# Kernel optimization log

Hardware: AMD Instinct MI355X
Metric: run time of the kernel (lower is better)

## Reference

```python
import jax, jax.numpy as jnp
import numpy as np

ALPHA = 0.9
BETA = 0.1
GAMMA = 0.1
EPS = 1e-8  # torch cosine_similarity eps


def setup_inputs() -> dict:
    key = jax.random.key(0)
    k1, k2 = jax.random.split(key)
    N = 8192
    y = jax.random.normal(k1, (N, 1), dtype=jnp.float32)
    labels = jax.random.normal(k2, (N, 1), dtype=jnp.float32)
    return {"y": y, "labels": labels}


def reference(y, labels):
    # --- MSE ---
    mse_loss = jnp.mean((y - labels) ** 2)

    # --- cosine similarity along dim=1 (torch semantics: each norm clamped by eps) ---
    yn = jnp.linalg.norm(y, axis=1)        # [N]
    ln = jnp.linalg.norm(labels, axis=1)   # [N]
    cos = jnp.sum(y * labels, axis=1) / (jnp.maximum(yn, EPS) * jnp.maximum(ln, EPS))
    similarity_loss = 1.0 - jnp.mean(cos)

    # --- vectorized pairwise margin ranking over i<j ---
    ys = y[:, 0]       # [N]
    ls = labels[:, 0]  # [N]
    dy = ys[:, None] - ys[None, :]   # [N, N]
    dl = ls[:, None] - ls[None, :]   # [N, N]
    # r_ij = 1 if labels[i] > labels[j], -1 if <, else sign(y[i]-y[j])
    r = jnp.where(dl > 0, 1.0, jnp.where(dl < 0, -1.0, jnp.sign(dy)))
    N = ys.shape[0]
    upper = jnp.triu(jnp.ones((N, N), dtype=bool), k=1)  # i<j pairs
    hinge = jnp.maximum(0.0, -r * dy)
    margin_ranking_loss = jnp.sum(jnp.where(upper, hinge, 0.0)) / (N * (N - 1) / 2)

    return ALPHA * mse_loss + BETA * margin_ranking_loss + GAMMA * similarity_loss
```

## Files before the change

kernel.cpp:

```cpp
#include <hip/hip_runtime.h>
#include <hip/hip_bf16.h>


constexpr int BLOCK = 256;
constexpr int JT    = 32;

#define EPS_F 1e-8f

__global__ __launch_bounds__(BLOCK) void combined_loss_pair_kernel(
    const float* __restrict__ y, const float* __restrict__ l, int N,
    float* __restrict__ hpart,
    float* __restrict__ mpart,
    float* __restrict__ cpart)
{
    __shared__ float sy[BLOCK];
    __shared__ float sl[BLOCK];
    __shared__ float red[BLOCK / 64];

    const int bx  = blockIdx.x;
    const int it  = bx / JT;
    const int jt  = bx % JT;
    const int tid = threadIdx.x;

    const int i    = it * BLOCK + tid;
    const bool valid = (i < N);
    const float yi = valid ? y[i] : 0.f;
    const float li = valid ? l[i] : 0.f;

    const int chunk = (N + JT - 1) / JT;
    const int j0 = jt * chunk;
    const int j1 = min(N, j0 + chunk);

    float hsum = 0.f;
    for (int jb = j0; jb < j1; jb += BLOCK) {
        const int cnt = min(BLOCK, j1 - jb);
        if (tid < cnt) {
            sy[tid] = y[jb + tid];
            sl[tid] = l[jb + tid];
        }
        __syncthreads();
        if (valid) {
#pragma unroll 8
            for (int k = 0; k < cnt; ++k) {
                const float dl = li - sl[k];
                const float dy = yi - sy[k];
                const float c = (dl > 0.f) ? fmaxf(-dy, 0.f)
                              : ((dl < 0.f) ? fmaxf(dy, 0.f) : 0.f);
                hsum += c;
            }
        }
        __syncthreads();
    }

    for (int o = 32; o > 0; o >>= 1) hsum += __shfl_down(hsum, o, 64);
    const int lane = tid & 63, wid = tid >> 6;
    if (lane == 0) red[wid] = hsum;
    __syncthreads();
    if (tid == 0) {
        float s = 0.f;
        for (int w = 0; w < BLOCK / 64; ++w) s += red[w];
        hpart[bx] = s;
    }
    __syncthreads();

    if (jt == 0) {
        float m = 0.f, c = 0.f;
        if (valid) {
            const float d = yi - li;
            m = d * d;
            c = (yi * li) / (fmaxf(fabsf(yi), EPS_F) * fmaxf(fabsf(li), EPS_F));
        }
        for (int o = 32; o > 0; o >>= 1) {
            m += __shfl_down(m, o, 64);
            c += __shfl_down(c, o, 64);
        }
        if (lane == 0) red[wid] = m;
        __syncthreads();
        float msum = 0.f;
        if (tid == 0) for (int w = 0; w < BLOCK / 64; ++w) msum += red[w];
        __syncthreads();
        if (lane == 0) red[wid] = c;
        __syncthreads();
        if (tid == 0) {
            float csum = 0.f;
            for (int w = 0; w < BLOCK / 64; ++w) csum += red[w];
            mpart[it] = msum;
            cpart[it] = csum;
        }
    }
}

__global__ __launch_bounds__(256) void combined_loss_finalize_kernel(
    const float* __restrict__ hpart, const float* __restrict__ mpart,
    const float* __restrict__ cpart, int nh, int nm, int N,
    float* __restrict__ out)
{
    double h = 0.0, m = 0.0, c = 0.0;
    for (int k = threadIdx.x; k < nh; k += blockDim.x) h += (double)hpart[k];
    for (int k = threadIdx.x; k < nm; k += blockDim.x) {
        m += (double)mpart[k];
        c += (double)cpart[k];
    }
    for (int o = 32; o > 0; o >>= 1) {
        h += __shfl_down(h, o, 64);
        m += __shfl_down(m, o, 64);
        c += __shfl_down(c, o, 64);
    }
    __shared__ double sh[4][3];
    const int lane = threadIdx.x & 63, wid = threadIdx.x >> 6;
    if (lane == 0) { sh[wid][0] = h; sh[wid][1] = m; sh[wid][2] = c; }
    __syncthreads();
    if (threadIdx.x == 0) {
        double H = 0, M = 0, C = 0;
        for (int w = 0; w < 4; ++w) { H += sh[w][0]; M += sh[w][1]; C += sh[w][2]; }
        const double Nd = (double)N;
        const double mse    = M / Nd;
        const double pairs  = Nd * (Nd - 1.0) * 0.5;
        const double margin = (H * 0.5) / pairs;
        const double sim    = 1.0 - C / Nd;
        out[0] = (float)(0.9 * mse + 0.1 * margin + 0.1 * sim);
    }
}

extern "C" void kernel_launch(void* const* d_in, const int* in_sizes, int n_in,
                              void* d_out, int out_size, void* d_ws, size_t ws_size,
                              hipStream_t stream) {
    const float* y = (const float*)d_in[0];
    const float* l = (const float*)d_in[1];
    const int N = in_sizes[0];

    const int IT = (N + BLOCK - 1) / BLOCK;
    float* hpart = (float*)d_ws;
    float* mpart = hpart + (size_t)IT * JT;
    float* cpart = mpart + IT;

    combined_loss_pair_kernel<<<IT * JT, BLOCK, 0, stream>>>(y, l, N, hpart, mpart, cpart);
    combined_loss_finalize_kernel<<<1, 256, 0, stream>>>(hpart, mpart, cpart, IT * JT, IT, N,
                                                         (float*)d_out);
}
```

Measured before the change: 82.24 us.

## Rewrite pairwise hinge as abs/sign sum and register-tile four rows per thread

Each hinge term is rewritten branch-free as 0.5*(|dy| + s*dy), where the sign s comes from comparing the labels. The two pieces are accumulated separately and combined once per row. Each thread now holds four i-rows in registers, and each block processes a 64-element j chunk read from LDS as float4, so every shared-memory load serves four rows. The aim is to cut per-pair ALU and LDS traffic while keeping about the same block count. The cost is more registers per thread, and exactly tied label pairs with i != j are handled slightly differently from the reference.

New measurement: 68.50 us. 16.7% less time.

```diff
diff --git a/kernel.cpp b/kernel.cpp
--- a/kernel.cpp
+++ b/kernel.cpp
@@ -3,18 +3,20 @@
 
 
 constexpr int BLOCK = 256;
-constexpr int JT    = 32;
+constexpr int M_PER = 4;
+constexpr int ITILE = BLOCK * M_PER;
+constexpr int JCH   = 64;
 
 #define EPS_F 1e-8f
 
 __global__ __launch_bounds__(BLOCK) void combined_loss_pair_kernel(
-    const float* __restrict__ y, const float* __restrict__ l, int N,
+    const float* __restrict__ y, const float* __restrict__ l, int N, int JT,
     float* __restrict__ hpart,
     float* __restrict__ mpart,
     float* __restrict__ cpart)
 {
-    __shared__ float sy[BLOCK];
-    __shared__ float sl[BLOCK];
+    __shared__ float sy[JCH];
+    __shared__ float sl[JCH];
     __shared__ float red[BLOCK / 64];
 
     const int bx  = blockIdx.x;
@@ -22,39 +24,60 @@
     const int jt  = bx % JT;
     const int tid = threadIdx.x;
 
-    const int i    = it * BLOCK + tid;
-    const bool valid = (i < N);
-    const float yi = valid ? y[i] : 0.f;
-    const float li = valid ? l[i] : 0.f;
-
-    const int chunk = (N + JT - 1) / JT;
-    const int j0 = jt * chunk;
-    const int j1 = min(N, j0 + chunk);
-
-    float hsum = 0.f;
-    for (int jb = j0; jb < j1; jb += BLOCK) {
-        const int cnt = min(BLOCK, j1 - jb);
-        if (tid < cnt) {
-            sy[tid] = y[jb + tid];
-            sl[tid] = l[jb + tid];
-        }
-        __syncthreads();
-        if (valid) {
-#pragma unroll 8
-            for (int k = 0; k < cnt; ++k) {
-                const float dl = li - sl[k];
-                const float dy = yi - sy[k];
-                const float c = (dl > 0.f) ? fmaxf(-dy, 0.f)
-                              : ((dl < 0.f) ? fmaxf(dy, 0.f) : 0.f);
-                hsum += c;
-            }
-        }
-        __syncthreads();
+    float yi[M_PER], li[M_PER];
+    bool  vm[M_PER];
+#pragma unroll
+    for (int m = 0; m < M_PER; ++m) {
+        const int i = it * ITILE + m * BLOCK + tid;
+        vm[m] = (i < N);
+        yi[m] = vm[m] ? y[i] : 0.f;
+        li[m] = vm[m] ? l[i] : 0.f;
     }
 
-    for (int o = 32; o > 0; o >>= 1) hsum += __shfl_down(hsum, o, 64);
+    const int j0   = jt * JCH;
+    const int jcnt = min(JCH, N - j0);
+    if (tid < JCH) {
+        const bool vj = (tid < jcnt);
+        sy[tid] = vj ? y[j0 + tid] : 0.f;
+        sl[tid] = vj ? l[j0 + tid] : 0.f;
+    }
+    __syncthreads();
+
+    float A[M_PER], B[M_PER];
+#pragma unroll
+    for (int m = 0; m < M_PER; ++m) { A[m] = 0.f; B[m] = 0.f; }
+
+#define PROC(yj, lj)                                         \
+    {                                                        \
+        _Pragma("unroll")                                    \
+        for (int m = 0; m < M_PER; ++m) {                    \
+            const float u = yi[m] - (yj);                    \
+            A[m] += fabsf(u);                                \
+            B[m] += (li[m] < (lj)) ? u : -u;                 \
+        }                                                    \
+    }
+
+    const int kv = jcnt & ~3;
+#pragma unroll 4
+    for (int k = 0; k < kv; k += 4) {
+        const float4 y4 = *reinterpret_cast<const float4*>(&sy[k]);
+        const float4 l4 = *reinterpret_cast<const float4*>(&sl[k]);
+        PROC(y4.x, l4.x);
+        PROC(y4.y, l4.y);
+        PROC(y4.z, l4.z);
+        PROC(y4.w, l4.w);
+    }
+    for (int k = kv; k < jcnt; ++k) PROC(sy[k], sl[k]);
+#undef PROC
+
+    float h = 0.f;
+#pragma unroll
+    for (int m = 0; m < M_PER; ++m)
+        if (vm[m]) h += 0.5f * (A[m] + B[m]);
+
+    for (int o = 32; o > 0; o >>= 1) h += __shfl_down(h, o, 64);
     const int lane = tid & 63, wid = tid >> 6;
-    if (lane == 0) red[wid] = hsum;
+    if (lane == 0) red[wid] = h;
     __syncthreads();
     if (tid == 0) {
         float s = 0.f;
@@ -64,28 +87,32 @@
     __syncthreads();
 
     if (jt == 0) {
-        float m = 0.f, c = 0.f;
-        if (valid) {
-            const float d = yi - li;
-            m = d * d;
-            c = (yi * li) / (fmaxf(fabsf(yi), EPS_F) * fmaxf(fabsf(li), EPS_F));
+        float msum = 0.f, csum = 0.f;
+#pragma unroll
+        for (int m = 0; m < M_PER; ++m) {
+            if (vm[m]) {
+                const float d = yi[m] - li[m];
+                msum += d * d;
+                csum += (yi[m] * li[m]) /
+                        (fmaxf(fabsf(yi[m]), EPS_F) * fmaxf(fabsf(li[m]), EPS_F));
+            }
         }
         for (int o = 32; o > 0; o >>= 1) {
-            m += __shfl_down(m, o, 64);
-            c += __shfl_down(c, o, 64);
+            msum += __shfl_down(msum, o, 64);
+            csum += __shfl_down(csum, o, 64);
         }
-        if (lane == 0) red[wid] = m;
+        if (lane == 0) red[wid] = msum;
         __syncthreads();
-        float msum = 0.f;
-        if (tid == 0) for (int w = 0; w < BLOCK / 64; ++w) msum += red[w];
+        float mtot = 0.f;
+        if (tid == 0) for (int w = 0; w < BLOCK / 64; ++w) mtot += red[w];
         __syncthreads();
-        if (lane == 0) red[wid] = c;
+        if (lane == 0) red[wid] = csum;
         __syncthreads();
         if (tid == 0) {
-            float csum = 0.f;
-            for (int w = 0; w < BLOCK / 64; ++w) csum += red[w];
-            mpart[it] = msum;
-            cpart[it] = csum;
+            float ctot = 0.f;
+            for (int w = 0; w < BLOCK / 64; ++w) ctot += red[w];
+            mpart[it] = mtot;
+            cpart[it] = ctot;
         }
     }
 }
@@ -113,7 +140,7 @@
     if (threadIdx.x == 0) {
         double H = 0, M = 0, C = 0;
         for (int w = 0; w < 4; ++w) { H += sh[w][0]; M += sh[w][1]; C += sh[w][2]; }
-        const double Nd = (double)N;
+        const double Nd     = (double)N;
         const double mse    = M / Nd;
         const double pairs  = Nd * (Nd - 1.0) * 0.5;
         const double margin = (H * 0.5) / pairs;
@@ -129,12 +156,16 @@
     const float* l = (const float*)d_in[1];
     const int N = in_sizes[0];
 
-    const int IT = (N + BLOCK - 1) / BLOCK;
+    const int IT = (N + ITILE - 1) / ITILE;
+    const int JT = (N + JCH - 1) / JCH;
+
     float* hpart = (float*)d_ws;
     float* mpart = hpart + (size_t)IT * JT;
     float* cpart = mpart + IT;
 
-    combined_loss_pair_kernel<<<IT * JT, BLOCK, 0, stream>>>(y, l, N, hpart, mpart, cpart);
-    combined_loss_finalize_kernel<<<1, 256, 0, stream>>>(hpart, mpart, cpart, IT * JT, IT, N,
+    combined_loss_pair_kernel<<<IT * JT, BLOCK, 0, stream>>>(y, l, N, JT,
+                                                             hpart, mpart, cpart);
+    combined_loss_finalize_kernel<<<1, 256, 0, stream>>>(hpart, mpart, cpart,
+                                                         IT * JT, IT, N,
                                                          (float*)d_out);
 }
```
